# Kernel tuning notes

Hardware: AMD Instinct MI355X
Metric: run time of the kernel (lower is better)

## Reference

```python
import jax, jax.numpy as jnp
import numpy as np

N_NODES = 100000
N_EDGES = 1600000
IN_DIM = 128
OUT_DIM = 64
SLOPE = 0.2


def setup_inputs() -> dict:
    key = jax.random.key(0)
    k1, k2, k3, k4 = jax.random.split(key, 4)
    h = jax.random.normal(k1, (N_NODES, IN_DIM), dtype=jnp.float32)
    W = jax.random.normal(k2, (OUT_DIM, IN_DIM), dtype=jnp.float32) * (1.0 / np.sqrt(IN_DIM))
    src = jax.random.randint(k3, (N_EDGES,), 0, N_NODES, dtype=jnp.int64)
    dst = jax.random.randint(k4, (N_EDGES,), 0, N_NODES, dtype=jnp.int64)
    return {"h": h, "W": W, "src": src, "dst": dst}


def reference(h, W, src, dst):
    n = h.shape[0]
    z = h @ W.T                                   # [N, out_dim]
    z_src = z[src]                                # [E, out_dim]
    z_dst = z[dst]                                # [E, out_dim]
    e = jax.nn.leaky_relu(jnp.sum(z_src * z_dst, axis=1), negative_slope=SLOPE)  # [E]
    # segment softmax over incoming edges of each destination node
    m = jax.ops.segment_max(e, dst, num_segments=n)        # [N], -inf for isolated nodes
    ex = jnp.exp(e - m[dst])                                # [E]
    denom = jax.ops.segment_sum(ex, dst, num_segments=n)    # [N]
    alpha = ex / denom[dst]                                 # [E]
    agg = jax.ops.segment_sum(alpha[:, None] * z_src, dst, num_segments=n)  # [N, out_dim]
    return jax.nn.elu(agg)
```

## Files before the change

kernel.cpp:

```cpp
#include <hip/hip_runtime.h>
#include <hip/hip_fp16.h>
#include <math.h>

#define SLOPE 0.2f
#define LOG2E 1.4426950408889634f

typedef _Float16 half8_t __attribute__((ext_vector_type(8)));
typedef _Float16 half2_t __attribute__((ext_vector_type(2)));
typedef float    f32x4_t __attribute__((ext_vector_type(4)));

__device__ __forceinline__ unsigned short pk_f16(float x) {
    return __half_as_ushort(__float2half(x));
}
__device__ __forceinline__ half2_t u2h2(unsigned int u) {
    union { unsigned int u; half2_t h; } c; c.u = u; return c.h;
}

__global__ __launch_bounds__(256) void wcvt_kernel(const float* __restrict__ W,
                                                   unsigned short* __restrict__ Wh,
                                                   int total4) {
    int i = blockIdx.x * 256 + threadIdx.x;
    if (i < total4) {
        float4 w = *(const float4*)(W + (size_t)i * 4);
        ushort4 o;
        o.x = pk_f16(w.x); o.y = pk_f16(w.y);
        o.z = pk_f16(w.z); o.w = pk_f16(w.w);
        *(ushort4*)(Wh + (size_t)i * 4) = o;
    }
}

__global__ __launch_bounds__(256, 8) void gemm_hist_kernel(const float* __restrict__ h,
                                                           const unsigned short* __restrict__ Wh,
                                                           unsigned short* __restrict__ zh,
                                                           const int* __restrict__ dst,
                                                           int* __restrict__ cnt8,
                                                           unsigned short* __restrict__ rank,
                                                           int n, int ne, int nGemm) {
    int r5 = blockIdx.x % 5;
    int g5 = blockIdx.x / 5;
    if (r5 == 4) {
        int* __restrict__ cnt = cnt8 + (size_t)(g5 & 7) * n;
        int i = g5 * 256 + threadIdx.x;
        int base = i * 4;
        if (base + 3 < ne) {
            int4 d = *(const int4*)(dst + base);
            unsigned int r0 = atomicAdd(&cnt[d.x], 1);
            unsigned int r1 = atomicAdd(&cnt[d.y], 1);
            unsigned int r2 = atomicAdd(&cnt[d.z], 1);
            unsigned int r3 = atomicAdd(&cnt[d.w], 1);
            uint2 packed;
            packed.x = (r1 << 16) | (r0 & 0xFFFF);
            packed.y = (r3 << 16) | (r2 & 0xFFFF);
            *(uint2*)(rank + base) = packed;
        } else if (base < ne) {
            for (int rr = base; rr < ne; rr++)
                rank[rr] = (unsigned short)atomicAdd(&cnt[dst[rr]], 1);
        }
        return;
    }

    int gemmIdx = g5 * 4 + r5;
    int n0 = gemmIdx * 16;
    if (n0 >= n) return;
    int lane = threadIdx.x & 63;
    int wave = threadIdx.x >> 6;
    int row = lane & 15;
    int grp = lane >> 4;
    int ch0 = wave * 16;

    const float* __restrict__ hp = h + (size_t)(n0 + row) * 128 + grp * 8;
    const unsigned short* __restrict__ wp = Wh + (size_t)(ch0 + row) * 128 + grp * 8;

    f32x4_t acc = {0.f, 0.f, 0.f, 0.f};
#pragma unroll
    for (int c = 0; c < 4; c++) {
        int kc = c * 32;
        float4 a0 = *(const float4*)(hp + kc);
        float4 a1 = *(const float4*)(hp + kc + 4);
        half8_t av;
        av[0] = (_Float16)a0.x; av[1] = (_Float16)a0.y;
        av[2] = (_Float16)a0.z; av[3] = (_Float16)a0.w;
        av[4] = (_Float16)a1.x; av[5] = (_Float16)a1.y;
        av[6] = (_Float16)a1.z; av[7] = (_Float16)a1.w;
        half8_t bv = *(const half8_t*)(wp + kc);
        acc = __builtin_amdgcn_mfma_f32_16x16x32_f16(av, bv, acc, 0, 0, 0);
    }
#pragma unroll
    for (int r = 0; r < 4; r++)
        zh[(size_t)(n0 + grp * 4 + r) * 64 + ch0 + row] = pk_f16(acc[r]);
}

__global__ __launch_bounds__(256) void scan1(const int* __restrict__ cnt8,
                                             int* __restrict__ starts,
                                             int* __restrict__ bsums, int n) {
    __shared__ int ls[256];
    int tbase = blockIdx.x * 4096 + threadIdx.x * 16;
    int tot[16];
#pragma unroll
    for (int k = 0; k < 16; k++) tot[k] = 0;
    if (tbase + 15 < n) {
#pragma unroll
        for (int c = 0; c < 8; c++) {
            const int* cp = cnt8 + (size_t)c * n + tbase;
#pragma unroll
            for (int q = 0; q < 4; q++) {
                int4 v = *(const int4*)(cp + q * 4);
                tot[q * 4 + 0] += v.x; tot[q * 4 + 1] += v.y;
                tot[q * 4 + 2] += v.z; tot[q * 4 + 3] += v.w;
            }
        }
    } else {
        for (int k = 0; k < 16; k++) {
            int idx = tbase + k;
            if (idx < n)
                for (int c = 0; c < 8; c++) tot[k] += cnt8[(size_t)c * n + idx];
        }
    }
    int s = 0;
#pragma unroll
    for (int k = 0; k < 16; k++) s += tot[k];
    ls[threadIdx.x] = s;
    __syncthreads();
    for (int off = 1; off < 256; off <<= 1) {
        int t = threadIdx.x >= off ? ls[threadIdx.x - off] : 0;
        __syncthreads();
        ls[threadIdx.x] += t;
        __syncthreads();
    }
    int run = ls[threadIdx.x] - s;
    if (threadIdx.x == 255) bsums[blockIdx.x] = ls[255];
#pragma unroll
    for (int k = 0; k < 16; k++) {
        int idx = tbase + k;
        if (idx < n) starts[idx] = run;
        run += tot[k];
    }
}

__global__ __launch_bounds__(256) void scan3(int* __restrict__ starts,
                                             const int* __restrict__ bsums,
                                             int* __restrict__ cnt8,
                                             int n, int ne) {
    __shared__ int base_s;
    int i = blockIdx.x * 256 + threadIdx.x;
    if (threadIdx.x == 0) {
        int reg = (int)(blockIdx.x >> 4);
        int s = 0;
        for (int b = 0; b < reg; b++) s += bsums[b];
        base_s = s;
        if (blockIdx.x == 0) starts[n] = ne;
    }
    __syncthreads();
    if (i >= n) return;
    int b = starts[i] + base_s;
    starts[i] = b;
#pragma unroll
    for (int c = 0; c < 8; c++) {
        size_t off = (size_t)c * n + i;
        int t = cnt8[off];
        cnt8[off] = b;
        b += t;
    }
}

__global__ __launch_bounds__(256) void scatter8_kernel(const int* __restrict__ src,
                                                       const int* __restrict__ dst,
                                                       const int* __restrict__ cnt8,
                                                       const unsigned short* __restrict__ rank,
                                                       int* __restrict__ csr_src,
                                                       int n, int ne) {
    int i = blockIdx.x * 256 + threadIdx.x;
    int base = i * 8;
    if (base + 7 < ne) {
        const int* __restrict__ cb = cnt8 + (size_t)((base >> 10) & 7) * n;
        int4 s0 = *(const int4*)(src + base),  s1 = *(const int4*)(src + base + 4);
        int4 d0 = *(const int4*)(dst + base),  d1 = *(const int4*)(dst + base + 4);
        uint4 rp = *(const uint4*)(rank + base);
        csr_src[cb[d0.x] + (rp.x & 0xFFFF)] = s0.x;
        csr_src[cb[d0.y] + (rp.x >> 16)]    = s0.y;
        csr_src[cb[d0.z] + (rp.y & 0xFFFF)] = s0.z;
        csr_src[cb[d0.w] + (rp.y >> 16)]    = s0.w;
        csr_src[cb[d1.x] + (rp.z & 0xFFFF)] = s1.x;
        csr_src[cb[d1.y] + (rp.z >> 16)]    = s1.y;
        csr_src[cb[d1.z] + (rp.w & 0xFFFF)] = s1.z;
        csr_src[cb[d1.w] + (rp.w >> 16)]    = s1.w;
    } else {
        for (int e = base; e < ne; e++) {
            const int* cb = cnt8 + (size_t)((e >> 10) & 7) * n;
            csr_src[cb[dst[e]] + rank[e]] = src[e];
        }
    }
}

__global__ __launch_bounds__(256) void fused_node(const unsigned short* __restrict__ zh,
                                                  const int* __restrict__ starts,
                                                  const int* __restrict__ csr_src,
                                                  float4* __restrict__ out4, int n) {
    int node = blockIdx.x * 4 + (threadIdx.x >> 6);
    if (node >= n) return;
    int lane = threadIdx.x & 63;
    int g4 = lane >> 4;
    int q4 = lane & 15;
    int rs = starts[node], re = starts[node + 1];

    const unsigned short* __restrict__ zdp = zh + (size_t)node * 64 + g4 * 8;
    half8_t bv0 = *(const half8_t*)(zdp);
    half8_t bv1 = *(const half8_t*)(zdp + 32);

    float m = -1e30f, denom = 0.f;
    float4 out = make_float4(0.f, 0.f, 0.f, 0.f);

    for (int c = rs; c < re; c += 64) {
        int j = c + lane;
        int sv = j < re ? csr_src[j] : 0;
        int cn = min(64, re - c);
        for (int t = 0; t * 16 < cn; t++) {
            int eidx = t * 16 + q4;
            int se = __shfl(sv, eidx < cn ? eidx : 0);
            const unsigned short* ap = zh + (size_t)se * 64 + g4 * 8;
            half8_t a0 = *(const half8_t*)(ap);
            half8_t a1 = *(const half8_t*)(ap + 32);
            f32x4_t acc = {0.f, 0.f, 0.f, 0.f};
            acc = __builtin_amdgcn_mfma_f32_16x16x32_f16(a0, bv0, acc, 0, 0, 0);
            acc = __builtin_amdgcn_mfma_f32_16x16x32_f16(a1, bv1, acc, 0, 0, 0);
            float e2[4];
            float cmax = -2e30f;
#pragma unroll
            for (int jj = 0; jj < 4; jj++) {
                float p = acc[jj];
                float e = fmaxf(p, SLOPE * p) * LOG2E;
                bool v = (t * 16 + g4 * 4 + jj) < cn;
                e2[jj] = v ? e : -2e30f;
                cmax = fmaxf(cmax, e2[jj]);
            }
            cmax = fmaxf(cmax, __shfl_xor(cmax, 16));
            cmax = fmaxf(cmax, __shfl_xor(cmax, 32));
            if (cmax > m) {
                float sc = exp2f(m - cmax);
                denom *= sc;
                out.x *= sc; out.y *= sc; out.z *= sc; out.w *= sc;
                m = cmax;
            }
            float ex[4];
#pragma unroll
            for (int jj = 0; jj < 4; jj++) {
                ex[jj] = exp2f(e2[jj] - m);
                denom += ex[jj];
            }
#pragma unroll
            for (int jj = 0; jj < 4; jj++) {
                int ei = t * 16 + g4 * 4 + jj;
                int sa = __shfl(sv, ei < cn ? ei : 0);
                uint2 w = *(const uint2*)(zh + (size_t)sa * 64 + q4 * 4);
                half2_t lo = u2h2(w.x), hi = u2h2(w.y);
                out.x = fmaf(ex[jj], (float)lo[0], out.x);
                out.y = fmaf(ex[jj], (float)lo[1], out.y);
                out.z = fmaf(ex[jj], (float)hi[0], out.z);
                out.w = fmaf(ex[jj], (float)hi[1], out.w);
            }
        }
    }
#pragma unroll
    for (int msk = 16; msk < 64; msk <<= 1) {
        denom += __shfl_xor(denom, msk);
        out.x += __shfl_xor(out.x, msk);
        out.y += __shfl_xor(out.y, msk);
        out.z += __shfl_xor(out.z, msk);
        out.w += __shfl_xor(out.w, msk);
    }
    if (g4 == 0) {
        float inv = denom > 0.f ? 1.f / denom : 0.f;
        float4 r;
        float x;
        x = out.x * inv; r.x = x > 0.f ? x : __expf(x) - 1.f;
        x = out.y * inv; r.y = x > 0.f ? x : __expf(x) - 1.f;
        x = out.z * inv; r.z = x > 0.f ? x : __expf(x) - 1.f;
        x = out.w * inv; r.w = x > 0.f ? x : __expf(x) - 1.f;
        out4[(size_t)node * 16 + q4] = r;
    }
}

extern "C" void kernel_launch(void* const* d_in, const int* in_sizes, int n_in,
                              void* d_out, int out_size, void* d_ws, size_t ws_size,
                              hipStream_t stream) {
    const float* h   = (const float*)d_in[0];
    const float* W   = (const float*)d_in[1];
    const int*   src = (const int*)d_in[2];
    const int*   dst = (const int*)d_in[3];
    int n  = in_sizes[0] / 128;
    int ne = in_sizes[2];

    unsigned short* zh      = (unsigned short*)d_ws;
    unsigned short* rank    = zh + (size_t)n * 64;
    int*            cnt8    = (int*)(rank + ne);
    int*            csr_src = cnt8 + (size_t)8 * n;
    unsigned short* Wh      = (unsigned short*)(csr_src + ne);
    int*            starts  = (int*)(Wh + 64 * 128);
    int*            bsums   = starts + ((n + 5) & ~3);

    int nGemm = (n + 15) / 16;
    int nbHist = (ne / 4 + 255) / 256;
    int nbTotal = nbHist * 5;
    int nb_scan = (n + 4095) / 4096;

    hipMemsetAsync(cnt8, 0, (size_t)8 * n * sizeof(int), stream);
    wcvt_kernel<<<(64 * 128 / 4 + 255) / 256, 256, 0, stream>>>(W, Wh, 64 * 128 / 4);
    gemm_hist_kernel<<<nbTotal, 256, 0, stream>>>(h, Wh, zh, dst, cnt8, rank,
                                                  n, ne, nGemm);
    scan1<<<nb_scan, 256, 0, stream>>>(cnt8, starts, bsums, n);
    scan3<<<(n + 255) / 256, 256, 0, stream>>>(starts, bsums, cnt8, n, ne);
    scatter8_kernel<<<(ne / 8 + 255) / 256, 256, 0, stream>>>(src, dst, cnt8,
                                                              rank, csr_src, n, ne);
    fused_node<<<(n + 3) / 4, 256, 0, stream>>>(zh, starts, csr_src,
                                                (float4*)d_out, n);
}
```

Baseline: 185.0 us.

## Fold W fp16 conversion into GEMM and rebalance GEMM/histogram block interleave

Removes the separate W-to-fp16 conversion kernel and has each GEMM wave load fp32 W and convert it inline, saving one launch and a workspace buffer. The interleaved fused kernel moves from 4 GEMM blocks plus 1 histogram block per group to 2 GEMM blocks plus 1 histogram block, with each histogram block now handling 2 edges per thread instead of 4. The scatter kernel's copy-selection shift is updated to match the new edge-per-block mapping. The trade-off is redundant W conversion in every GEMM block and more histogram blocks, each doing fewer atomics.

```diff
diff --git a/kernel.cpp b/kernel.cpp
--- a/kernel.cpp
+++ b/kernel.cpp
@@ -16,50 +16,31 @@
     union { unsigned int u; half2_t h; } c; c.u = u; return c.h;
 }
 
-__global__ __launch_bounds__(256) void wcvt_kernel(const float* __restrict__ W,
-                                                   unsigned short* __restrict__ Wh,
-                                                   int total4) {
-    int i = blockIdx.x * 256 + threadIdx.x;
-    if (i < total4) {
-        float4 w = *(const float4*)(W + (size_t)i * 4);
-        ushort4 o;
-        o.x = pk_f16(w.x); o.y = pk_f16(w.y);
-        o.z = pk_f16(w.z); o.w = pk_f16(w.w);
-        *(ushort4*)(Wh + (size_t)i * 4) = o;
-    }
-}
-
 __global__ __launch_bounds__(256, 8) void gemm_hist_kernel(const float* __restrict__ h,
-                                                           const unsigned short* __restrict__ Wh,
+                                                           const float* __restrict__ W,
                                                            unsigned short* __restrict__ zh,
                                                            const int* __restrict__ dst,
                                                            int* __restrict__ cnt8,
                                                            unsigned short* __restrict__ rank,
-                                                           int n, int ne, int nGemm) {
-    int r5 = blockIdx.x % 5;
-    int g5 = blockIdx.x / 5;
-    if (r5 == 4) {
-        int* __restrict__ cnt = cnt8 + (size_t)(g5 & 7) * n;
-        int i = g5 * 256 + threadIdx.x;
-        int base = i * 4;
-        if (base + 3 < ne) {
-            int4 d = *(const int4*)(dst + base);
+                                                           int n, int ne) {
+    int r3 = blockIdx.x % 3;
+    int g3 = blockIdx.x / 3;
+    if (r3 == 2) {
+        int* __restrict__ cnt = cnt8 + (size_t)(g3 & 7) * n;
+        int i = g3 * 256 + threadIdx.x;
+        int base = i * 2;
+        if (base + 1 < ne) {
+            int2 d = *(const int2*)(dst + base);
             unsigned int r0 = atomicAdd(&cnt[d.x], 1);
             unsigned int r1 = atomicAdd(&cnt[d.y], 1);
-            unsigned int r2 = atomicAdd(&cnt[d.z], 1);
-            unsigned int r3 = atomicAdd(&cnt[d.w], 1);
-            uint2 packed;
-            packed.x = (r1 << 16) | (r0 & 0xFFFF);
-            packed.y = (r3 << 16) | (r2 & 0xFFFF);
-            *(uint2*)(rank + base) = packed;
+            *(unsigned int*)(rank + base) = (r1 << 16) | (r0 & 0xFFFF);
         } else if (base < ne) {
-            for (int rr = base; rr < ne; rr++)
-                rank[rr] = (unsigned short)atomicAdd(&cnt[dst[rr]], 1);
+            rank[base] = (unsigned short)atomicAdd(&cnt[dst[base]], 1);
         }
         return;
     }
 
-    int gemmIdx = g5 * 4 + r5;
+    int gemmIdx = g3 * 2 + r3;
     int n0 = gemmIdx * 16;
     if (n0 >= n) return;
     int lane = threadIdx.x & 63;
@@ -69,7 +50,7 @@
     int ch0 = wave * 16;
 
     const float* __restrict__ hp = h + (size_t)(n0 + row) * 128 + grp * 8;
-    const unsigned short* __restrict__ wp = Wh + (size_t)(ch0 + row) * 128 + grp * 8;
+    const float* __restrict__ wp = W + (size_t)(ch0 + row) * 128 + grp * 8;
 
     f32x4_t acc = {0.f, 0.f, 0.f, 0.f};
 #pragma unroll
@@ -82,7 +63,13 @@
         av[2] = (_Float16)a0.z; av[3] = (_Float16)a0.w;
         av[4] = (_Float16)a1.x; av[5] = (_Float16)a1.y;
         av[6] = (_Float16)a1.z; av[7] = (_Float16)a1.w;
-        half8_t bv = *(const half8_t*)(wp + kc);
+        float4 b0 = *(const float4*)(wp + kc);
+        float4 b1 = *(const float4*)(wp + kc + 4);
+        half8_t bv;
+        bv[0] = (_Float16)b0.x; bv[1] = (_Float16)b0.y;
+        bv[2] = (_Float16)b0.z; bv[3] = (_Float16)b0.w;
+        bv[4] = (_Float16)b1.x; bv[5] = (_Float16)b1.y;
+        bv[6] = (_Float16)b1.z; bv[7] = (_Float16)b1.w;
         acc = __builtin_amdgcn_mfma_f32_16x16x32_f16(av, bv, acc, 0, 0, 0);
     }
 #pragma unroll
@@ -172,7 +159,7 @@
     int i = blockIdx.x * 256 + threadIdx.x;
     int base = i * 8;
     if (base + 7 < ne) {
-        const int* __restrict__ cb = cnt8 + (size_t)((base >> 10) & 7) * n;
+        const int* __restrict__ cb = cnt8 + (size_t)((base >> 9) & 7) * n;
         int4 s0 = *(const int4*)(src + base),  s1 = *(const int4*)(src + base + 4);
         int4 d0 = *(const int4*)(dst + base),  d1 = *(const int4*)(dst + base + 4);
         uint4 rp = *(const uint4*)(rank + base);
@@ -186,7 +173,7 @@
         csr_src[cb[d1.w] + (rp.w >> 16)]    = s1.w;
     } else {
         for (int e = base; e < ne; e++) {
-            const int* cb = cnt8 + (size_t)((e >> 10) & 7) * n;
+            const int* cb = cnt8 + (size_t)((e >> 9) & 7) * n;
             csr_src[cb[dst[e]] + rank[e]] = src[e];
         }
     }
@@ -294,19 +281,15 @@
     unsigned short* rank    = zh + (size_t)n * 64;
     int*            cnt8    = (int*)(rank + ne);
     int*            csr_src = cnt8 + (size_t)8 * n;
-    unsigned short* Wh      = (unsigned short*)(csr_src + ne);
-    int*            starts  = (int*)(Wh + 64 * 128);
+    int*            starts  = csr_src + ne;
     int*            bsums   = starts + ((n + 5) & ~3);
 
-    int nGemm = (n + 15) / 16;
-    int nbHist = (ne / 4 + 255) / 256;
-    int nbTotal = nbHist * 5;
+    int nbHist = (ne / 2 + 255) / 256;
+    int nbTotal = (nbHist + 1) * 3;
     int nb_scan = (n + 4095) / 4096;
 
     hipMemsetAsync(cnt8, 0, (size_t)8 * n * sizeof(int), stream);
-    wcvt_kernel<<<(64 * 128 / 4 + 255) / 256, 256, 0, stream>>>(W, Wh, 64 * 128 / 4);
-    gemm_hist_kernel<<<nbTotal, 256, 0, stream>>>(h, Wh, zh, dst, cnt8, rank,
-                                                  n, ne, nGemm);
+    gemm_hist_kernel<<<nbTotal, 256, 0, stream>>>(h, W, zh, dst, cnt8, rank, n, ne);
     scan1<<<nb_scan, 256, 0, stream>>>(cnt8, starts, bsums, n);
     scan3<<<(n + 255) / 256, 256, 0, stream>>>(starts, bsums, cnt8, n, ne);
     scatter8_kernel<<<(ne / 8 + 255) / 256, 256, 0, stream>>>(src, dst, cnt8,
```

New measurement: 183.1 us. Within noise of the previous version (-1.0%).
